# Kernel optimization log

Measured on AMD Instinct MI355X. Metric: run time of the kernel, lower is better.

## Reference

```python
import jax, jax.numpy as jnp
import numpy as np

D_IN, H1, H2, B, K = 128, 128, 64, 262144, 4

def _mk(key, shape):
    return jax.random.normal(key, shape, dtype=jnp.float32) * 0.05

def setup_inputs() -> dict:
    key = jax.random.key(0)
    ks = jax.random.split(key, 40)
    inp = {
        'x': jax.random.normal(ks[0], (B, 96), dtype=jnp.float32),
        'u': jax.random.normal(ks[1], (B, 32), dtype=jnp.float32),
        'mix_factor': jax.random.uniform(ks[2], (1,), dtype=jnp.float32),
        'teacher_P': jax.random.uniform(ks[3], (K,), dtype=jnp.float32),
    }
    # main critic params (torch Linear: W [out,in], b [out])
    dims = [(H1, D_IN), (H1, H1), (H2, H1), (1, H2)] * 2  # l1..l4, l5..l8
    for i, (o, ii) in enumerate(dims):
        inp[f'W{i+1}'] = _mk(ks[4 + 2 * i], (o, ii))
        inp[f'b{i+1}'] = _mk(ks[5 + 2 * i], (o,))
    # stacked teacher params (K teachers), only l1,l2,l3,l5,l6,l7 are used
    tdims = {'1': (H1, D_IN), '2': (H1, H1), '3': (H2, H1), '5': (H1, D_IN), '6': (H1, H1), '7': (H2, H1)}
    j = 20
    for name, (o, ii) in tdims.items():
        inp[f'tW{name}'] = _mk(ks[j], (K, o, ii)); j += 1
        inp[f'tb{name}'] = _mk(ks[j], (K, o)); j += 1
    return inp

def reference(x, u, mix_factor, teacher_P, W1, b1, W2, b2, W3, b3, W4, b4, W5, b5, W6, b6, W7, b7, W8, b8, tW1, tb1, tW2, tb2, tW3, tb3, tW5, tb5, tW6, tb6, tW7, tb7):
    m = mix_factor  # [1], broadcasts
    P = teacher_P   # [K]
    xu = jnp.concatenate([x, u], axis=1)  # [B, 128]

    lin = lambda h, W, b: h @ W.T + b
    # teacher linear on shared input [B,I] -> [K,B,O]
    tlin0 = lambda h, W, b: jnp.einsum('bi,koi->kbo', h, W) + b[:, None, :]
    # teacher linear on per-teacher streams [K,B,I] -> [K,B,O]
    tlin = lambda h, W, b: jnp.einsum('kbi,koi->kbo', h, W) + b[:, None, :]
    mixsum = lambda ht: jnp.einsum('kbo,k->bo', ht, P)

    def head(W_a, b_a, W_b, b_b, W_c, b_c, W_d, b_d, tWa, tba, tWb, tbb, tWc, tbc):
        ht = tlin0(xu, tWa, tba)                                   # [K,B,128]
        h = jax.nn.relu(lin(xu, W_a, b_a) * (1 - m) + mixsum(ht) * m)
        ht = jax.nn.relu(ht)
        ht2 = tlin(ht, tWb, tbb)
        h = jax.nn.relu(lin(h, W_b, b_b) * (1 - m) + mixsum(ht2) * m)
        ht2 = jax.nn.relu(ht2)
        ht3 = tlin(ht2, tWc, tbc)
        h = jax.nn.relu(lin(h, W_c, b_c) * (1 - m) + mixsum(ht3) * m)
        return lin(h, W_d, b_d)                                    # [B,1]

    x1 = head(W1, b1, W2, b2, W3, b3, W4, b4, tW1, tb1, tW2, tb2, tW3, tb3)
    x2 = head(W5, b5, W6, b6, W7, b7, W8, b8, tW5, tb5, tW6, tb6, tW7, tb7)
    return (x1, x2)
```

## Files before the change

### kernel.cpp

```cpp
#include <hip/hip_runtime.h>
#include <hip/hip_bf16.h>
#include <stdint.h>

#define B_TOTAL 262144
#define TB 64
#define SLOT 16384
#define BUF1 81920
#define LDS_BYTES 163840
#define HEAD_W 204800

typedef short v8s __attribute__((ext_vector_type(8)));
typedef float v4f __attribute__((ext_vector_type(4)));

union Frag { uint4 q; uint32_t d[4]; v8s v; };

__device__ __forceinline__ uint32_t pack2(float a, float b) {
    union { __hip_bfloat162 h; uint32_t u; } p;
    p.h = __float22bfloat162_rn(make_float2(a, b));
    return p.u;
}


struct KParams {
    const float* x; const float* u; const float* mix; const float* P;
    const float* mb[6];
    const float* tb[6];
    const float* Wout[2];
    const float* bout[2];
    const unsigned short* wbf;
    float* out;
};

struct PrepParams { const float* src[12]; unsigned short* dst; };

__global__ __launch_bounds__(256) void prep_kernel(PrepParams pp) {
    const int ends[12] = {16384,81920,98304,163840,172032,204800,
                          221184,286720,303104,368640,376832,409600};
    int gi = (blockIdx.x * 256 + threadIdx.x) * 4;
    if (gi >= 409600) return;
    int s = 0;
    #pragma unroll
    for (int i = 0; i < 12; ++i) { if (gi >= ends[i]) s = i + 1; }
    int base = (s == 0) ? 0 : ends[s - 1];
    const float4 f = *(const float4*)(pp.src[s] + (gi - base));
    *(uint2*)(pp.dst + gi) = make_uint2(pack2(f.x, f.y), pack2(f.z, f.w));
}

__device__ __forceinline__ void stage_xu(char* lds, const float* x, const float* u,
                                         int rowBase, int tid)
{
    for (int G = tid; G < 1024; G += 512) {
        const int row = G >> 4;
        const int gg  = G & 15;
        const int grow = rowBase + row;
        float4 fa, fb;
        if (gg < 12) {
            const float* s2 = x + grow * 96 + gg * 8;
            fa = *(const float4*)s2; fb = *(const float4*)(s2 + 4);
        } else {
            const float* s2 = u + grow * 32 + (gg - 12) * 8;
            fa = *(const float4*)s2; fb = *(const float4*)(s2 + 4);
        }
        *(uint4*)(lds + row * 256 + ((gg ^ (row & 15)) << 4)) =
            make_uint4(pack2(fa.x, fa.y), pack2(fa.z, fa.w),
                       pack2(fb.x, fb.y), pack2(fb.z, fb.w));
    }
}

struct WPre { Frag w[20]; float4 mB; float4 tB[4]; };

template<int N>
__device__ __forceinline__ WPre preload(const unsigned short* W,
        const float* mbias, const float* tbias, int lane, int wave)
{
    WPre r;
    const int l15  = lane & 15;
    const int quad = lane >> 4;
    const int colBase = (N == 64) ? ((wave >> 1) << 4) : (wave << 4);
    const unsigned short* wRow = W + (colBase + l15) * 128 + quad * 8;
    #pragma unroll
    for (int s = 0; s < 5; ++s)
        #pragma unroll
        for (int ks = 0; ks < 4; ++ks)
            r.w[s * 4 + ks].q = *(const uint4*)(wRow + s * (N * 128) + ks * 32);
    const int obase = colBase + quad * 4;
    r.mB = *(const float4*)(mbias + obase);
    #pragma unroll
    for (int s = 0; s < 4; ++s)
        r.tB[s] = *(const float4*)(tbias + s * N + obase);
    return r;
}

template<bool SHARED_IN, int N>
__device__ __forceinline__ void compute(char* lds, int inOff, int outOff,
        const WPre& wp, float c0, const float* cP, int lane, int wave,
        const float* Wout, float* pgrid)
{
    constexpr bool FINAL = (N == 64);
    constexpr int NBT = FINAL ? 2 : 4;
    const int l15  = lane & 15;
    const int quad = lane >> 4;
    const int colBase = FINAL ? ((wave >> 1) << 4) : (wave << 4);
    const int btBase  = FINAL ? ((wave & 1) << 1) : 0;

    v4f acc[5][NBT];
    #pragma unroll
    for (int s = 0; s < 5; ++s)
        #pragma unroll
        for (int bt = 0; bt < NBT; ++bt)
            acc[s][bt] = (v4f){0.f, 0.f, 0.f, 0.f};

    #pragma unroll
    for (int ks = 0; ks < 4; ++ks) {
        const int gg = ks * 4 + quad;
        Frag xS[NBT];
        if constexpr (SHARED_IN) {
            #pragma unroll
            for (int bt = 0; bt < NBT; ++bt) {
                const int row = (btBase + bt) * 16 + l15;
                xS[bt].q = *(const uint4*)(lds + inOff + row * 256 + ((gg ^ (row & 15)) << 4));
            }
        }
        #pragma unroll
        for (int s = 0; s < 5; ++s) {
            Frag xF[NBT];
            if constexpr (!SHARED_IN) {
                #pragma unroll
                for (int bt = 0; bt < NBT; ++bt) {
                    const int row = (btBase + bt) * 16 + l15;
                    xF[bt].q = *(const uint4*)(lds + inOff + s * SLOT + row * 256
                                               + ((gg ^ (row & 15)) << 4));
                }
            }
            #pragma unroll
            for (int bt = 0; bt < NBT; ++bt)
                acc[s][bt] = __builtin_amdgcn_mfma_f32_16x16x32_bf16(
                    wp.w[s * 4 + ks].v, (SHARED_IN ? xS[bt].v : xF[bt].v),
                    acc[s][bt], 0, 0, 0);
        }
    }

    const int obase = colBase + quad * 4;

    if constexpr (!FINAL) {
        #pragma unroll
        for (int bt = 0; bt < 4; ++bt) {
            const int row = bt * 16 + l15;
            char* ab = lds + outOff + row * 256 + (((obase >> 3) ^ (row & 15)) << 4)
                       + ((obase & 7) << 1);
            float vr[4];
            vr[0] = c0 * (acc[0][bt][0] + wp.mB.x);
            vr[1] = c0 * (acc[0][bt][1] + wp.mB.y);
            vr[2] = c0 * (acc[0][bt][2] + wp.mB.z);
            vr[3] = c0 * (acc[0][bt][3] + wp.mB.w);
            uint2 tw[4];
            #pragma unroll
            for (int s = 0; s < 4; ++s) {
                float t0 = acc[s + 1][bt][0] + wp.tB[s].x;
                float t1 = acc[s + 1][bt][1] + wp.tB[s].y;
                float t2 = acc[s + 1][bt][2] + wp.tB[s].z;
                float t3 = acc[s + 1][bt][3] + wp.tB[s].w;
                vr[0] = fmaf(cP[s], t0, vr[0]);
                vr[1] = fmaf(cP[s], t1, vr[1]);
                vr[2] = fmaf(cP[s], t2, vr[2]);
                vr[3] = fmaf(cP[s], t3, vr[3]);
                tw[s] = make_uint2(pack2(fmaxf(t0, 0.f), fmaxf(t1, 0.f)),
                                   pack2(fmaxf(t2, 0.f), fmaxf(t3, 0.f)));
            }
            *(uint2*)ab = make_uint2(pack2(fmaxf(vr[0], 0.f), fmaxf(vr[1], 0.f)),
                                     pack2(fmaxf(vr[2], 0.f), fmaxf(vr[3], 0.f)));
            #pragma unroll
            for (int s = 0; s < 4; ++s)
                *(uint2*)(ab + (s + 1) * SLOT) = tw[s];
        }
    } else {
        const float4 wo = *(const float4*)(Wout + obase);
        float psum[NBT];
        #pragma unroll
        for (int j = 0; j < NBT; ++j) {
            float vr[4];
            vr[0] = c0 * (acc[0][j][0] + wp.mB.x);
            vr[1] = c0 * (acc[0][j][1] + wp.mB.y);
            vr[2] = c0 * (acc[0][j][2] + wp.mB.z);
            vr[3] = c0 * (acc[0][j][3] + wp.mB.w);
            #pragma unroll
            for (int s = 0; s < 4; ++s) {
                vr[0] = fmaf(cP[s], acc[s + 1][j][0] + wp.tB[s].x, vr[0]);
                vr[1] = fmaf(cP[s], acc[s + 1][j][1] + wp.tB[s].y, vr[1]);
                vr[2] = fmaf(cP[s], acc[s + 1][j][2] + wp.tB[s].z, vr[2]);
                vr[3] = fmaf(cP[s], acc[s + 1][j][3] + wp.tB[s].w, vr[3]);
            }
            float pp = fmaxf(vr[0], 0.f) * wo.x + fmaxf(vr[1], 0.f) * wo.y
                     + fmaxf(vr[2], 0.f) * wo.z + fmaxf(vr[3], 0.f) * wo.w;
            pp += __shfl_xor(pp, 16);
            pp += __shfl_xor(pp, 32);
            psum[j] = pp;
        }
        if (lane < 16) {
            #pragma unroll
            for (int j = 0; j < NBT; ++j)
                pgrid[(wave >> 1) * 64 + (btBase + j) * 16 + lane] = psum[j];
        }
    }
}

extern "C" __global__ __launch_bounds__(512, 2)
void critic_kernel(KParams p)
{
    extern __shared__ char lds[];
    const int tid  = threadIdx.x;
    const int lane = tid & 63;
    const int wave = tid >> 6;
    const int rowBase = blockIdx.x * TB;

    const float m  = p.mix[0];
    const float c0 = 1.f - m;
    float cP[4];
    #pragma unroll
    for (int k = 0; k < 4; ++k) cP[k] = m * p.P[k];

    stage_xu(lds, p.x, p.u, rowBase, tid);

    #pragma unroll 1
    for (int head = 0; head < 2; ++head) {
        const unsigned short* wb = p.wbf + head * HEAD_W;
        const int hb = head * 3;

        WPre w1 = preload<128>(wb, p.mb[hb + 0], p.tb[hb + 0], lane, wave);
        __syncthreads();
        compute<true, 128>(lds, 0, BUF1, w1, c0, cP, lane, wave, nullptr, nullptr);

        WPre w2 = preload<128>(wb + 81920, p.mb[hb + 1], p.tb[hb + 1], lane, wave);
        __syncthreads();
        compute<false, 128>(lds, BUF1, 0, w2, c0, cP, lane, wave, nullptr, nullptr);

        WPre w3 = preload<64>(wb + 163840, p.mb[hb + 2], p.tb[hb + 2], lane, wave);
        __syncthreads();
        compute<false, 64>(lds, 0, 0, w3, c0, cP, lane, wave,
                           p.Wout[head], (float*)(lds + BUF1));
        __syncthreads();

        if (tid < 64) {
            const float* pg = (const float*)(lds + BUF1);
            p.out[head * B_TOTAL + rowBase + tid] =
                p.bout[head][0] + pg[tid] + pg[64 + tid] + pg[128 + tid] + pg[192 + tid];
        }
        if (head == 0) {
            stage_xu(lds, p.x, p.u, rowBase, tid);
        }
    }
}

extern "C" void kernel_launch(void* const* d_in, const int* in_sizes, int n_in,
                              void* d_out, int out_size, void* d_ws, size_t ws_size,
                              hipStream_t stream)
{
    (void)in_sizes; (void)n_in; (void)out_size; (void)ws_size;

    PrepParams pp;
    const int sidx[12] = {4, 20, 6, 22, 8, 24, 12, 26, 14, 28, 16, 30};
    for (int i = 0; i < 12; ++i) pp.src[i] = (const float*)d_in[sidx[i]];
    pp.dst = (unsigned short*)d_ws;

    KParams kp;
    kp.x = (const float*)d_in[0];  kp.u = (const float*)d_in[1];
    kp.mix = (const float*)d_in[2]; kp.P = (const float*)d_in[3];
    const int mbi[6] = {5, 7, 9, 13, 15, 17};
    const int tbi[6] = {21, 23, 25, 27, 29, 31};
    for (int i = 0; i < 6; ++i) {
        kp.mb[i] = (const float*)d_in[mbi[i]];
        kp.tb[i] = (const float*)d_in[tbi[i]];
    }
    kp.Wout[0] = (const float*)d_in[10]; kp.Wout[1] = (const float*)d_in[18];
    kp.bout[0] = (const float*)d_in[11]; kp.bout[1] = (const float*)d_in[19];
    kp.wbf = (const unsigned short*)d_ws;
    kp.out = (float*)d_out;

    (void)hipFuncSetAttribute((const void*)critic_kernel,
                              hipFuncAttributeMaxDynamicSharedMemorySize, LDS_BYTES);

    hipLaunchKernelGGL(prep_kernel, dim3(400), dim3(256), 0, stream, pp);
    hipLaunchKernelGGL(critic_kernel, dim3(4096), dim3(512), LDS_BYTES, stream, kp);
}
```

Before: 846.7 us.

## Halve row tile and stream weights per slice to raise occupancy

Shrinks the per-block row tile from 64 to 32, halving LDS use so up to four 512-thread blocks can be resident, and raises launch bounds accordingly. Weight fragments are no longer preloaded into registers before the barrier; they are loaded from global memory slice by slice inside the compute loop, and input fragments for all k-steps are loaded up front. This cuts register pressure and improves latency hiding, but each weight is now reused across half as many rows, which doubles weight reads from L2 and MFMA work per weight load. Weight loads also no longer overlap the barrier wait.

```diff
diff --git a/kernel.cpp b/kernel.cpp
--- a/kernel.cpp
+++ b/kernel.cpp
@@ -3,10 +3,10 @@
 #include <stdint.h>
 
 #define B_TOTAL 262144
-#define TB 64
-#define SLOT 16384
-#define BUF1 81920
-#define LDS_BYTES 163840
+#define TB 32
+#define SLOT 8192
+#define BUF1 40960
+#define LDS_BYTES 81920
 #define HEAD_W 204800
 
 typedef short v8s __attribute__((ext_vector_type(8)));
@@ -49,59 +49,36 @@
 __device__ __forceinline__ void stage_xu(char* lds, const float* x, const float* u,
                                          int rowBase, int tid)
 {
-    for (int G = tid; G < 1024; G += 512) {
-        const int row = G >> 4;
-        const int gg  = G & 15;
-        const int grow = rowBase + row;
-        float4 fa, fb;
-        if (gg < 12) {
-            const float* s2 = x + grow * 96 + gg * 8;
-            fa = *(const float4*)s2; fb = *(const float4*)(s2 + 4);
-        } else {
-            const float* s2 = u + grow * 32 + (gg - 12) * 8;
-            fa = *(const float4*)s2; fb = *(const float4*)(s2 + 4);
-        }
-        *(uint4*)(lds + row * 256 + ((gg ^ (row & 15)) << 4)) =
-            make_uint4(pack2(fa.x, fa.y), pack2(fa.z, fa.w),
-                       pack2(fb.x, fb.y), pack2(fb.z, fb.w));
-    }
-}
-
-struct WPre { Frag w[20]; float4 mB; float4 tB[4]; };
-
-template<int N>
-__device__ __forceinline__ WPre preload(const unsigned short* W,
-        const float* mbias, const float* tbias, int lane, int wave)
-{
-    WPre r;
-    const int l15  = lane & 15;
-    const int quad = lane >> 4;
-    const int colBase = (N == 64) ? ((wave >> 1) << 4) : (wave << 4);
-    const unsigned short* wRow = W + (colBase + l15) * 128 + quad * 8;
-    #pragma unroll
-    for (int s = 0; s < 5; ++s)
-        #pragma unroll
-        for (int ks = 0; ks < 4; ++ks)
-            r.w[s * 4 + ks].q = *(const uint4*)(wRow + s * (N * 128) + ks * 32);
-    const int obase = colBase + quad * 4;
-    r.mB = *(const float4*)(mbias + obase);
-    #pragma unroll
-    for (int s = 0; s < 4; ++s)
-        r.tB[s] = *(const float4*)(tbias + s * N + obase);
-    return r;
+    const int row = tid >> 4;
+    const int gg  = tid & 15;
+    const int grow = rowBase + row;
+    float4 fa, fb;
+    if (gg < 12) {
+        const float* s2 = x + grow * 96 + gg * 8;
+        fa = *(const float4*)s2; fb = *(const float4*)(s2 + 4);
+    } else {
+        const float* s2 = u + grow * 32 + (gg - 12) * 8;
+        fa = *(const float4*)s2; fb = *(const float4*)(s2 + 4);
+    }
+    *(uint4*)(lds + row * 256 + ((gg ^ (row & 15)) << 4)) =
+        make_uint4(pack2(fa.x, fa.y), pack2(fa.z, fa.w),
+                   pack2(fb.x, fb.y), pack2(fb.z, fb.w));
 }
 
 template<bool SHARED_IN, int N>
 __device__ __forceinline__ void compute(char* lds, int inOff, int outOff,
-        const WPre& wp, float c0, const float* cP, int lane, int wave,
+        const unsigned short* W, const float* mbias, const float* tbias,
+        float c0, const float* cP, int lane, int wave,
         const float* Wout, float* pgrid)
 {
     constexpr bool FINAL = (N == 64);
-    constexpr int NBT = FINAL ? 2 : 4;
+    constexpr int NBT = FINAL ? 1 : 2;
     const int l15  = lane & 15;
     const int quad = lane >> 4;
     const int colBase = FINAL ? ((wave >> 1) << 4) : (wave << 4);
-    const int btBase  = FINAL ? ((wave & 1) << 1) : 0;
+    const int btBase  = FINAL ? (wave & 1) : 0;
+
+    const unsigned short* wRow = W + (colBase + l15) * 128 + quad * 8;
 
     v4f acc[5][NBT];
     #pragma unroll
@@ -110,56 +87,73 @@
         for (int bt = 0; bt < NBT; ++bt)
             acc[s][bt] = (v4f){0.f, 0.f, 0.f, 0.f};
 
-    #pragma unroll
-    for (int ks = 0; ks < 4; ++ks) {
-        const int gg = ks * 4 + quad;
-        Frag xS[NBT];
-        if constexpr (SHARED_IN) {
+    Frag xS[4][NBT];
+    if constexpr (SHARED_IN) {
+        #pragma unroll
+        for (int ks = 0; ks < 4; ++ks) {
+            const int gg = ks * 4 + quad;
             #pragma unroll
             for (int bt = 0; bt < NBT; ++bt) {
                 const int row = (btBase + bt) * 16 + l15;
-                xS[bt].q = *(const uint4*)(lds + inOff + row * 256 + ((gg ^ (row & 15)) << 4));
+                xS[ks][bt].q = *(const uint4*)(lds + inOff + row * 256
+                                               + ((gg ^ (row & 15)) << 4));
             }
         }
-        #pragma unroll
-        for (int s = 0; s < 5; ++s) {
-            Frag xF[NBT];
-            if constexpr (!SHARED_IN) {
+    }
+
+    #pragma unroll
+    for (int s = 0; s < 5; ++s) {
+        Frag wf[4];
+        #pragma unroll
+        for (int ks = 0; ks < 4; ++ks)
+            wf[ks].q = *(const uint4*)(wRow + s * (N * 128) + ks * 32);
+        Frag xF[4][NBT];
+        if constexpr (!SHARED_IN) {
+            #pragma unroll
+            for (int ks = 0; ks < 4; ++ks) {
+                const int gg = ks * 4 + quad;
                 #pragma unroll
                 for (int bt = 0; bt < NBT; ++bt) {
                     const int row = (btBase + bt) * 16 + l15;
-                    xF[bt].q = *(const uint4*)(lds + inOff + s * SLOT + row * 256
-                                               + ((gg ^ (row & 15)) << 4));
+                    xF[ks][bt].q = *(const uint4*)(lds + inOff + s * SLOT
+                                    + row * 256 + ((gg ^ (row & 15)) << 4));
                 }
             }
+        }
+        #pragma unroll
+        for (int ks = 0; ks < 4; ++ks)
             #pragma unroll
             for (int bt = 0; bt < NBT; ++bt)
                 acc[s][bt] = __builtin_amdgcn_mfma_f32_16x16x32_bf16(
-                    wp.w[s * 4 + ks].v, (SHARED_IN ? xS[bt].v : xF[bt].v),
+                    wf[ks].v, (SHARED_IN ? xS[ks][bt].v : xF[ks][bt].v),
                     acc[s][bt], 0, 0, 0);
-        }
     }
 
     const int obase = colBase + quad * 4;
+    const float4 mB = *(const float4*)(mbias + obase);
+    float4 tB[4];
+    #pragma unroll
+    for (int s = 0; s < 4; ++s)
+        tB[s] = *(const float4*)(tbias + s * N + obase);
 
     if constexpr (!FINAL) {
         #pragma unroll
-        for (int bt = 0; bt < 4; ++bt) {
+        for (int bt = 0; bt < NBT; ++bt) {
             const int row = bt * 16 + l15;
             char* ab = lds + outOff + row * 256 + (((obase >> 3) ^ (row & 15)) << 4)
                        + ((obase & 7) << 1);
             float vr[4];
-            vr[0] = c0 * (acc[0][bt][0] + wp.mB.x);
-            vr[1] = c0 * (acc[0][bt][1] + wp.mB.y);
-            vr[2] = c0 * (acc[0][bt][2] + wp.mB.z);
-            vr[3] = c0 * (acc[0][bt][3] + wp.mB.w);
+            vr[0] = c0 * (acc[0][bt][0] + mB.x);
+            vr[1] = c0 * (acc[0][bt][1] + mB.y);
+            vr[2] = c0 * (acc[0][bt][2] + mB.z);
+            vr[3] = c0 * (acc[0][bt][3] + mB.w);
             uint2 tw[4];
             #pragma unroll
             for (int s = 0; s < 4; ++s) {
-                float t0 = acc[s + 1][bt][0] + wp.tB[s].x;
-                float t1 = acc[s + 1][bt][1] + wp.tB[s].y;
-                float t2 = acc[s + 1][bt][2] + wp.tB[s].z;
-                float t3 = acc[s + 1][bt][3] + wp.tB[s].w;
+                float t0 = acc[s + 1][bt][0] + tB[s].x;
+                float t1 = acc[s + 1][bt][1] + tB[s].y;
+                float t2 = acc[s + 1][bt][2] + tB[s].z;
+                float t3 = acc[s + 1][bt][3] + tB[s].w;
                 vr[0] = fmaf(cP[s], t0, vr[0]);
                 vr[1] = fmaf(cP[s], t1, vr[1]);
                 vr[2] = fmaf(cP[s], t2, vr[2]);
@@ -175,36 +169,28 @@
         }
     } else {
         const float4 wo = *(const float4*)(Wout + obase);
-        float psum[NBT];
-        #pragma unroll
-        for (int j = 0; j < NBT; ++j) {
-            float vr[4];
-            vr[0] = c0 * (acc[0][j][0] + wp.mB.x);
-            vr[1] = c0 * (acc[0][j][1] + wp.mB.y);
-            vr[2] = c0 * (acc[0][j][2] + wp.mB.z);
-            vr[3] = c0 * (acc[0][j][3] + wp.mB.w);
-            #pragma unroll
-            for (int s = 0; s < 4; ++s) {
-                vr[0] = fmaf(cP[s], acc[s + 1][j][0] + wp.tB[s].x, vr[0]);
-                vr[1] = fmaf(cP[s], acc[s + 1][j][1] + wp.tB[s].y, vr[1]);
-                vr[2] = fmaf(cP[s], acc[s + 1][j][2] + wp.tB[s].z, vr[2]);
-                vr[3] = fmaf(cP[s], acc[s + 1][j][3] + wp.tB[s].w, vr[3]);
-            }
-            float pp = fmaxf(vr[0], 0.f) * wo.x + fmaxf(vr[1], 0.f) * wo.y
-                     + fmaxf(vr[2], 0.f) * wo.z + fmaxf(vr[3], 0.f) * wo.w;
-            pp += __shfl_xor(pp, 16);
-            pp += __shfl_xor(pp, 32);
-            psum[j] = pp;
-        }
-        if (lane < 16) {
-            #pragma unroll
-            for (int j = 0; j < NBT; ++j)
-                pgrid[(wave >> 1) * 64 + (btBase + j) * 16 + lane] = psum[j];
-        }
-    }
-}
-
-extern "C" __global__ __launch_bounds__(512, 2)
+        float vr[4];
+        vr[0] = c0 * (acc[0][0][0] + mB.x);
+        vr[1] = c0 * (acc[0][0][1] + mB.y);
+        vr[2] = c0 * (acc[0][0][2] + mB.z);
+        vr[3] = c0 * (acc[0][0][3] + mB.w);
+        #pragma unroll
+        for (int s = 0; s < 4; ++s) {
+            vr[0] = fmaf(cP[s], acc[s + 1][0][0] + tB[s].x, vr[0]);
+            vr[1] = fmaf(cP[s], acc[s + 1][0][1] + tB[s].y, vr[1]);
+            vr[2] = fmaf(cP[s], acc[s + 1][0][2] + tB[s].z, vr[2]);
+            vr[3] = fmaf(cP[s], acc[s + 1][0][3] + tB[s].w, vr[3]);
+        }
+        float pp = fmaxf(vr[0], 0.f) * wo.x + fmaxf(vr[1], 0.f) * wo.y
+                 + fmaxf(vr[2], 0.f) * wo.z + fmaxf(vr[3], 0.f) * wo.w;
+        pp += __shfl_xor(pp, 16);
+        pp += __shfl_xor(pp, 32);
+        if (lane < 16)
+            pgrid[(wave >> 1) * 32 + btBase * 16 + lane] = pp;
+    }
+}
+
+extern "C" __global__ __launch_bounds__(512, 4)
 void critic_kernel(KParams p)
 {
     extern __shared__ char lds[];
@@ -226,24 +212,21 @@
         const unsigned short* wb = p.wbf + head * HEAD_W;
         const int hb = head * 3;
 
-        WPre w1 = preload<128>(wb, p.mb[hb + 0], p.tb[hb + 0], lane, wave);
-        __syncthreads();
-        compute<true, 128>(lds, 0, BUF1, w1, c0, cP, lane, wave, nullptr, nullptr);
-
-        WPre w2 = preload<128>(wb + 81920, p.mb[hb + 1], p.tb[hb + 1], lane, wave);
-        __syncthreads();
-        compute<false, 128>(lds, BUF1, 0, w2, c0, cP, lane, wave, nullptr, nullptr);
-
-        WPre w3 = preload<64>(wb + 163840, p.mb[hb + 2], p.tb[hb + 2], lane, wave);
-        __syncthreads();
-        compute<false, 64>(lds, 0, 0, w3, c0, cP, lane, wave,
-                           p.Wout[head], (float*)(lds + BUF1));
-        __syncthreads();
-
-        if (tid < 64) {
+        __syncthreads();
+        compute<true, 128>(lds, 0, BUF1, wb, p.mb[hb + 0], p.tb[hb + 0],
+                           c0, cP, lane, wave, nullptr, nullptr);
+        __syncthreads();
+        compute<false, 128>(lds, BUF1, 0, wb + 81920, p.mb[hb + 1], p.tb[hb + 1],
+                            c0, cP, lane, wave, nullptr, nullptr);
+        __syncthreads();
+        compute<false, 64>(lds, 0, 0, wb + 163840, p.mb[hb + 2], p.tb[hb + 2],
+                           c0, cP, lane, wave, p.Wout[head], (float*)(lds + BUF1));
+        __syncthreads();
+
+        if (tid < 32) {
             const float* pg = (const float*)(lds + BUF1);
             p.out[head * B_TOTAL + rowBase + tid] =
-                p.bout[head][0] + pg[tid] + pg[64 + tid] + pg[128 + tid] + pg[192 + tid];
+                p.bout[head][0] + pg[tid] + pg[32 + tid] + pg[64 + tid] + pg[96 + tid];
         }
         if (head == 0) {
             stage_xu(lds, p.x, p.u, rowBase, tid);
@@ -280,5 +263,5 @@
                               hipFuncAttributeMaxDynamicSharedMemorySize, LDS_BYTES);
 
     hipLaunchKernelGGL(prep_kernel, dim3(400), dim3(256), 0, stream, pp);
-    hipLaunchKernelGGL(critic_kernel, dim3(4096), dim3(512), LDS_BYTES, stream, kp);
-}
+    hipLaunchKernelGGL(critic_kernel, dim3(B_TOTAL / TB), dim3(512), LDS_BYTES, stream, kp);
+}
```

Result: slower. 1.190 ms (+40.5%).

## Interleave activation slots per row and fold biases into accumulator init

Applied to the files above, without the earlier changes.

Changes the LDS layout from separate 16 KB slots per stream to per-row records of 2560 bytes, where each row holds ten 256-byte slots (input, main and teacher streams, double-buffered). Addresses are precomputed per lane with template offsets, which cuts integer address arithmetic in the MFMA loops. Biases are now loaded into the accumulators at init, which removes the bias adds in the epilogue. The pgrid scratch moves to offset 1280 inside row 0, and the risk is new bank-conflict patterns from the 2560-byte row stride.

```diff
diff --git a/kernel.cpp b/kernel.cpp
--- a/kernel.cpp
+++ b/kernel.cpp
@@ -4,8 +4,7 @@
 
 #define B_TOTAL 262144
 #define TB 64
-#define SLOT 16384
-#define BUF1 81920
+#define RECORD 2560
 #define LDS_BYTES 163840
 #define HEAD_W 204800
 
@@ -61,7 +60,7 @@
             const float* s2 = u + grow * 32 + (gg - 12) * 8;
             fa = *(const float4*)s2; fb = *(const float4*)(s2 + 4);
         }
-        *(uint4*)(lds + row * 256 + ((gg ^ (row & 15)) << 4)) =
+        *(uint4*)(lds + row * RECORD + ((gg ^ (row & 15)) << 4)) =
             make_uint4(pack2(fa.x, fa.y), pack2(fa.z, fa.w),
                        pack2(fb.x, fb.y), pack2(fb.z, fb.w));
     }
@@ -91,8 +90,8 @@
     return r;
 }
 
-template<bool SHARED_IN, int N>
-__device__ __forceinline__ void compute(char* lds, int inOff, int outOff,
+template<bool SHARED_IN, int N, int INS, int OUTS>
+__device__ __forceinline__ void compute(char* lds,
         const WPre& wp, float c0, const float* cP, int lane, int wave,
         const float* Wout, float* pgrid)
 {
@@ -103,22 +102,40 @@
     const int colBase = FINAL ? ((wave >> 1) << 4) : (wave << 4);
     const int btBase  = FINAL ? ((wave & 1) << 1) : 0;
 
+    const uint32_t rb = (uint32_t)l15 * RECORD + ((uint32_t)l15 << 4);
+    uint32_t rA[4];
+    #pragma unroll
+    for (int ks = 0; ks < 4; ++ks)
+        rA[ks] = rb ^ (uint32_t)(((ks << 2) | quad) << 4);
+    if constexpr (FINAL) {
+        const uint32_t bo = (uint32_t)btBase * 40960u;
+        #pragma unroll
+        for (int ks = 0; ks < 4; ++ks) rA[ks] += bo;
+    }
+    uint32_t rB[4];
+    if constexpr (!FINAL) {
+        #pragma unroll
+        for (int ks = 0; ks < 4; ++ks) rB[ks] = rA[ks] + 2u * 40960u;
+    }
+
     v4f acc[5][NBT];
     #pragma unroll
-    for (int s = 0; s < 5; ++s)
-        #pragma unroll
-        for (int bt = 0; bt < NBT; ++bt)
-            acc[s][bt] = (v4f){0.f, 0.f, 0.f, 0.f};
+    for (int bt = 0; bt < NBT; ++bt) {
+        acc[0][bt] = (v4f){wp.mB.x, wp.mB.y, wp.mB.z, wp.mB.w};
+        #pragma unroll
+        for (int s = 0; s < 4; ++s)
+            acc[s + 1][bt] = (v4f){wp.tB[s].x, wp.tB[s].y, wp.tB[s].z, wp.tB[s].w};
+    }
 
     #pragma unroll
     for (int ks = 0; ks < 4; ++ks) {
-        const int gg = ks * 4 + quad;
         Frag xS[NBT];
         if constexpr (SHARED_IN) {
             #pragma unroll
             for (int bt = 0; bt < NBT; ++bt) {
-                const int row = (btBase + bt) * 16 + l15;
-                xS[bt].q = *(const uint4*)(lds + inOff + row * 256 + ((gg ^ (row & 15)) << 4));
+                const uint32_t a = (bt < 2) ? (rA[ks] + (uint32_t)(bt * 40960 + INS * 256))
+                                            : (rB[ks] + (uint32_t)((bt - 2) * 40960 + INS * 256));
+                xS[bt].q = *(const uint4*)(lds + a);
             }
         }
         #pragma unroll
@@ -127,9 +144,9 @@
             if constexpr (!SHARED_IN) {
                 #pragma unroll
                 for (int bt = 0; bt < NBT; ++bt) {
-                    const int row = (btBase + bt) * 16 + l15;
-                    xF[bt].q = *(const uint4*)(lds + inOff + s * SLOT + row * 256
-                                               + ((gg ^ (row & 15)) << 4));
+                    const uint32_t a = (bt < 2) ? (rA[ks] + (uint32_t)(bt * 40960 + (INS + s) * 256))
+                                                : (rB[ks] + (uint32_t)((bt - 2) * 40960 + (INS + s) * 256));
+                    xF[bt].q = *(const uint4*)(lds + a);
                 }
             }
             #pragma unroll
@@ -140,26 +157,26 @@
         }
     }
 
-    const int obase = colBase + quad * 4;
+    const int obase = colBase + (quad << 2);
 
     if constexpr (!FINAL) {
+        const int ocg = (colBase >> 3) + (quad >> 1);
+        const uint32_t w0 = (rb ^ ((uint32_t)ocg << 4)) + (uint32_t)((quad & 1) << 3);
         #pragma unroll
         for (int bt = 0; bt < 4; ++bt) {
-            const int row = bt * 16 + l15;
-            char* ab = lds + outOff + row * 256 + (((obase >> 3) ^ (row & 15)) << 4)
-                       + ((obase & 7) << 1);
+            char* ab = lds + (w0 + (uint32_t)(bt * 40960));
             float vr[4];
-            vr[0] = c0 * (acc[0][bt][0] + wp.mB.x);
-            vr[1] = c0 * (acc[0][bt][1] + wp.mB.y);
-            vr[2] = c0 * (acc[0][bt][2] + wp.mB.z);
-            vr[3] = c0 * (acc[0][bt][3] + wp.mB.w);
+            vr[0] = c0 * acc[0][bt][0];
+            vr[1] = c0 * acc[0][bt][1];
+            vr[2] = c0 * acc[0][bt][2];
+            vr[3] = c0 * acc[0][bt][3];
             uint2 tw[4];
             #pragma unroll
             for (int s = 0; s < 4; ++s) {
-                float t0 = acc[s + 1][bt][0] + wp.tB[s].x;
-                float t1 = acc[s + 1][bt][1] + wp.tB[s].y;
-                float t2 = acc[s + 1][bt][2] + wp.tB[s].z;
-                float t3 = acc[s + 1][bt][3] + wp.tB[s].w;
+                const float t0 = acc[s + 1][bt][0];
+                const float t1 = acc[s + 1][bt][1];
+                const float t2 = acc[s + 1][bt][2];
+                const float t3 = acc[s + 1][bt][3];
                 vr[0] = fmaf(cP[s], t0, vr[0]);
                 vr[1] = fmaf(cP[s], t1, vr[1]);
                 vr[2] = fmaf(cP[s], t2, vr[2]);
@@ -167,11 +184,12 @@
                 tw[s] = make_uint2(pack2(fmaxf(t0, 0.f), fmaxf(t1, 0.f)),
                                    pack2(fmaxf(t2, 0.f), fmaxf(t3, 0.f)));
             }
-            *(uint2*)ab = make_uint2(pack2(fmaxf(vr[0], 0.f), fmaxf(vr[1], 0.f)),
-                                     pack2(fmaxf(vr[2], 0.f), fmaxf(vr[3], 0.f)));
+            *(uint2*)(ab + OUTS * 256) =
+                make_uint2(pack2(fmaxf(vr[0], 0.f), fmaxf(vr[1], 0.f)),
+                           pack2(fmaxf(vr[2], 0.f), fmaxf(vr[3], 0.f)));
             #pragma unroll
             for (int s = 0; s < 4; ++s)
-                *(uint2*)(ab + (s + 1) * SLOT) = tw[s];
+                *(uint2*)(ab + (OUTS + 1 + s) * 256) = tw[s];
         }
     } else {
         const float4 wo = *(const float4*)(Wout + obase);
@@ -179,16 +197,16 @@
         #pragma unroll
         for (int j = 0; j < NBT; ++j) {
             float vr[4];
-            vr[0] = c0 * (acc[0][j][0] + wp.mB.x);
-            vr[1] = c0 * (acc[0][j][1] + wp.mB.y);
-            vr[2] = c0 * (acc[0][j][2] + wp.mB.z);
-            vr[3] = c0 * (acc[0][j][3] + wp.mB.w);
+            vr[0] = c0 * acc[0][j][0];
+            vr[1] = c0 * acc[0][j][1];
+            vr[2] = c0 * acc[0][j][2];
+            vr[3] = c0 * acc[0][j][3];
             #pragma unroll
             for (int s = 0; s < 4; ++s) {
-                vr[0] = fmaf(cP[s], acc[s + 1][j][0] + wp.tB[s].x, vr[0]);
-                vr[1] = fmaf(cP[s], acc[s + 1][j][1] + wp.tB[s].y, vr[1]);
-                vr[2] = fmaf(cP[s], acc[s + 1][j][2] + wp.tB[s].z, vr[2]);
-                vr[3] = fmaf(cP[s], acc[s + 1][j][3] + wp.tB[s].w, vr[3]);
+                vr[0] = fmaf(cP[s], acc[s + 1][j][0], vr[0]);
+                vr[1] = fmaf(cP[s], acc[s + 1][j][1], vr[1]);
+                vr[2] = fmaf(cP[s], acc[s + 1][j][2], vr[2]);
+                vr[3] = fmaf(cP[s], acc[s + 1][j][3], vr[3]);
             }
             float pp = fmaxf(vr[0], 0.f) * wo.x + fmaxf(vr[1], 0.f) * wo.y
                      + fmaxf(vr[2], 0.f) * wo.z + fmaxf(vr[3], 0.f) * wo.w;
@@ -228,20 +246,20 @@
 
         WPre w1 = preload<128>(wb, p.mb[hb + 0], p.tb[hb + 0], lane, wave);
         __syncthreads();
-        compute<true, 128>(lds, 0, BUF1, w1, c0, cP, lane, wave, nullptr, nullptr);
+        compute<true, 128, 0, 5>(lds, w1, c0, cP, lane, wave, nullptr, nullptr);
 
         WPre w2 = preload<128>(wb + 81920, p.mb[hb + 1], p.tb[hb + 1], lane, wave);
         __syncthreads();
-        compute<false, 128>(lds, BUF1, 0, w2, c0, cP, lane, wave, nullptr, nullptr);
+        compute<false, 128, 5, 0>(lds, w2, c0, cP, lane, wave, nullptr, nullptr);
 
         WPre w3 = preload<64>(wb + 163840, p.mb[hb + 2], p.tb[hb + 2], lane, wave);
         __syncthreads();
-        compute<false, 64>(lds, 0, 0, w3, c0, cP, lane, wave,
-                           p.Wout[head], (float*)(lds + BUF1));
+        compute<false, 64, 0, 0>(lds, w3, c0, cP, lane, wave,
+                                 p.Wout[head], (float*)(lds + 1280));
         __syncthreads();
 
         if (tid < 64) {
-            const float* pg = (const float*)(lds + BUF1);
+            const float* pg = (const float*)(lds + 1280);
             p.out[head * B_TOTAL + rowBase + tid] =
                 p.bout[head][0] + pg[tid] + pg[64 + tid] + pg[128 + tid] + pg[192 + tid];
         }
@@ -280,5 +298,5 @@
                               hipFuncAttributeMaxDynamicSharedMemorySize, LDS_BYTES);
 
     hipLaunchKernelGGL(prep_kernel, dim3(400), dim3(256), 0, stream, pp);
-    hipLaunchKernelGGL(critic_kernel, dim3(4096), dim3(512), LDS_BYTES, stream, kp);
-}
+    hipLaunchKernelGGL(critic_kernel, dim3(B_TOTAL / TB), dim3(512), LDS_BYTES, stream, kp);
+}
```

After: 860.3 us. No clear change (+1.6%).
